# Performance work log

Hardware: AMD Instinct MI355X
Metric: run time of the kernel (lower is better)

## Reference

```python
import jax, jax.numpy as jnp
import numpy as np

FFT_LIST = [32, 64, 128]
C_IN = 64
C_OUT = 96
C_OUT_PER = C_OUT // len(FFT_LIST)  # 32
BASIC = FFT_LIST[1]                 # base kernel defined at fft=64 -> 33 bins
ALPHA = 0.2                         # tf.nn.leaky_relu default


def setup_inputs() -> dict:
    key = jax.random.key(0)
    k1, k2, k3, k4 = jax.random.split(key, 4)
    B, T = 8, 8192
    bins0 = BASIC // 2 + 1
    return {
        "x": jax.random.normal(k1, (B, T, C_IN), dtype=jnp.float32),
        "kernel_r": jax.random.normal(k2, (1, 1, bins0, C_IN * C_OUT_PER), dtype=jnp.float32) * 0.05,
        "kernel_i": jax.random.normal(k3, (1, 1, bins0, C_IN * C_OUT_PER), dtype=jnp.float32) * 0.05,
        "bias_r": jax.random.normal(k4, (C_OUT,), dtype=jnp.float32) * 0.05,
    }


def _resize_bins(k, bins):
    # tf.image.resize on [1, H=1, W=bins0, C]: bilinear along W, half-pixel, no antialias
    if bins == k.shape[2]:
        return k
    return jax.image.resize(k, (1, 1, bins, k.shape[3]), method="linear", antialias=False)


def _leaky(v):
    return jax.nn.leaky_relu(v, negative_slope=ALPHA)


def reference(x, kernel_r, kernel_i, bias_r):
    B, T, _ = x.shape
    xc = jnp.transpose(x, (0, 2, 1))  # [B, C_in, T]
    outs = []
    for fft_n in FFT_LIST:
        frames = T // fft_n
        bins = fft_n // 2 + 1
        # non-overlapping STFT with no window == reshape + rfft
        xf = jnp.fft.rfft(xc.reshape(B, C_IN, frames, fft_n), axis=-1)  # [B, Cin, F, K] complex64
        kr = _resize_bins(kernel_r, bins)
        ki = _resize_bins(kernel_i, bins)
        kern = (kr + 1j * ki).reshape(bins, C_IN, C_OUT_PER).astype(jnp.complex64)  # [K, Cin, Cout]
        # per-frequency-bin complex matmul over c_in (fuses tile+mul+reduce_sum)
        y = jnp.einsum("bcfk,kco->bofk", xf, kern)  # [B, Cout, F, K]
        # act_domain == 'freq': leaky relu on real and imag parts
        y = _leaky(jnp.real(y)) + 1j * _leaky(jnp.imag(y))
        # inverse STFT (step == length, no window) == irfft + reshape
        yt = jnp.fft.irfft(y, n=fft_n, axis=-1)            # [B, Cout, F, fft_n]
        yt = yt.reshape(B, C_OUT_PER, T)                    # [B, Cout, T]
        outs.append(jnp.transpose(yt, (0, 2, 1)))           # [B, T, Cout]
    out = jnp.concatenate(outs, axis=2)                     # [B, T, C_OUT]
    out = out + bias_r                                      # bias_add(real(bias))
    return out
```

## Files before the change

kernel.cpp:

```cpp
#include <hip/hip_runtime.h>
#include <stdint.h>

#define T_SZ 8192
#define NCH 96

typedef __attribute__((ext_vector_type(8))) short s8v;
typedef __attribute__((ext_vector_type(4))) float f4v;

__device__ __forceinline__ float lo_bf(uint32_t u){ return __uint_as_float(u << 16); }
__device__ __forceinline__ float hi_bf(uint32_t u){ return __uint_as_float(u & 0xffff0000u); }
__device__ __forceinline__ uint32_t f2bf(float f){
    uint32_t u = __float_as_uint(f);
    return (u + 0x7fffu + ((u >> 16) & 1u)) >> 16;
}
__device__ __forceinline__ uint32_t pk2(float a, float b){ return f2bf(a) | (f2bf(b) << 16); }

#define WS_TOTAL_PAIRS 235520
#define WD_OFF    942080
#define WD_ELEMS  27264
#define WA_OFF    996608
#define WA_ELEMS  30464
#define WD64_U16   1920
#define WD128_U16  7680
#define WA64_U16   2304
#define WA128_U16  8960
#define WE_OFF   1057536
#define WE_U32    471040
#define XF32W    4194304
#define XF64W   14680064
#define XF128W  25165824
#define Y32W    35651584
#define Y64W    41943040
#define Y128W   50331648
#define WS_WIDE 58720256

__global__ void prep_full(const float* __restrict__ kr, const float* __restrict__ ki,
                          char* __restrict__ ws)
{
    int idx = blockIdx.x * 256 + threadIdx.x;
    if (idx < WE_U32) {
        int g = idx >> 12, r = idx & 4095;
        int row = r >> 6, c = r & 63;
        int o = row & 31, half = row >> 5;
        int bins, k;
        if (g < 17)      { bins = 17; k = g; }
        else if (g < 50) { bins = 33; k = g - 17; }
        else             { bins = 65; k = g - 50; }
        float s  = (k + 0.5f) * (33.0f / bins) - 0.5f;
        float fl = floorf(s);
        float w1 = s - fl;
        int i0 = min(max((int)fl, 0), 32);
        int i1 = min(max((int)fl + 1, 0), 32);
        int co = c * 32 + o;
        float r0 = kr[i0 * 2048 + co], r1 = kr[i1 * 2048 + co];
        float q0 = ki[i0 * 2048 + co], q1 = ki[i1 * 2048 + co];
        int N = bins * 2 - 2;
        float wk = (k == 0 || k == bins - 1) ? (1.0f / N) : (2.0f / N);
        float vr = fmaf(w1, r1 - r0, r0) * wk;
        float vi = fmaf(w1, q1 - q0, q0) * wk;
        ((uint32_t*)(ws + WE_OFF))[idx] = half ? pk2(vi, vr) : pk2(vr, -vi);
        return;
    }
    int e = idx - WE_U32;
    if (e < WD_ELEMS) {
        int N, NP, base;
        if (e < 1920)      { N = 32;  NP = 40;  base = 0; }
        else if (e < 7680) { N = 64;  NP = 72;  base = WD64_U16;  e -= 1920; }
        else               { N = 128; NP = 136; base = WD128_U16; e -= 7680; }
        int m = e / NP, t = e % NP;
        float v = 0.f;
        if (t < N && m < N + 2) {
            float ang = 6.2831853071795864769f * (float)(((m >> 1) * t) & (N - 1)) / (float)N;
            v = (m & 1) ? -sinf(ang) : cosf(ang);
        }
        ((unsigned short*)(ws + WD_OFF))[base + e] = (unsigned short)f2bf(v);
        return;
    }
    e -= WD_ELEMS;
    if (e < WA_ELEMS) {
        int N, S3, base;
        if (e < 2304)      { N = 32;  S3 = 72;  base = 0; }
        else if (e < 8960) { N = 64;  S3 = 104; base = WA64_U16;  e -= 2304; }
        else               { N = 128; S3 = 168; base = WA128_U16; e -= 8960; }
        int t = e / S3, kk = e % S3;
        int BINS = N / 2 + 1;
        float v = 0.f;
        if (kk < BINS)
            v = cosf(6.2831853071795864769f * (float)((kk * t) & (N - 1)) / (float)N);
        else if (kk < N + 2)
            v = -sinf(6.2831853071795864769f * (float)(((kk - BINS) * t) & (N - 1)) / (float)N);
        ((unsigned short*)(ws + WA_OFF))[base + e] = (unsigned short)f2bf(v);
    }
}

__global__ void prep_resize(const float* __restrict__ kr, const float* __restrict__ ki,
                            uint32_t* __restrict__ wsu)
{
    int idx = blockIdx.x * 256 + threadIdx.x;
    if (idx >= WS_TOTAL_PAIRS) return;
    int bins, rem = idx;
    if (rem < 17 * 2048)      { bins = 17; }
    else if (rem < 50 * 2048) { bins = 33; rem -= 17 * 2048; }
    else                      { bins = 65; rem -= 50 * 2048; }
    int k = rem >> 11, co = rem & 2047;
    float s  = (k + 0.5f) * (33.0f / bins) - 0.5f;
    float fl = floorf(s);
    float w1 = s - fl;
    int i0 = min(max((int)fl, 0), 32);
    int i1 = min(max((int)fl + 1, 0), 32);
    float r0 = kr[i0 * 2048 + co], r1 = kr[i1 * 2048 + co];
    float q0 = ki[i0 * 2048 + co], q1 = ki[i1 * 2048 + co];
    wsu[idx] = pk2(fmaf(w1, r1 - r0, r0), fmaf(w1, q1 - q0, q0));
}

__device__ __forceinline__ s8v ldfr(const unsigned short* p, int stride, int row0, int k0){
    int lane = threadIdx.x & 63;
    return *(const s8v*)(p + (row0 + (lane & 15)) * stride + k0 + ((lane >> 4) << 3));
}

template<int N, int NTW>
__device__ __forceinline__ void k1w_branch(const unsigned short* __restrict__ W,
        const unsigned short* __restrict__ xT, uint32_t* __restrict__ xfp, int b, int w)
{
    constexpr int BINS = N/2+1, M2 = 2*BINS, MPAD = ((M2+15)/16)*16;
    constexpr int MT = MPAD/16, KS = N/32, NP = N+8;
    constexpr int F = 128/N, FRAMES = 8192/N, BF = 8*FRAMES;
    const int tid = threadIdx.x, wv = tid >> 6, lane = tid & 63;
    const int nt0 = wv * NTW, cl = lane & 15, kl = (lane >> 4) << 3, rg = (lane >> 4) * 4;

    f4v acc[MT][NTW];
    #pragma unroll
    for (int mt = 0; mt < MT; ++mt)
        #pragma unroll
        for (int nw = 0; nw < NTW; ++nw) { f4v zz = {0.f,0.f,0.f,0.f}; acc[mt][nw] = zz; }

    for (int ks = 0; ks < KS; ++ks) {
        s8v a[MT];
        #pragma unroll
        for (int mt = 0; mt < MT; ++mt) a[mt] = ldfr(W, NP, mt*16, ks*32);
        #pragma unroll
        for (int nw = 0; nw < NTW; ++nw) {
            int rowb = (nt0+nw)*16 + cl;
            s8v bb = *(const s8v*)(xT + (rowb & 63)*136 + (rowb >> 6)*N + ks*32 + kl);
            #pragma unroll
            for (int mt = 0; mt < MT; ++mt)
                acc[mt][nw] = __builtin_amdgcn_mfma_f32_16x16x32_bf16(a[mt], bb, acc[mt][nw], 0, 0, 0);
        }
    }
    #pragma unroll
    for (int mt = 0; mt < MT; ++mt)
      #pragma unroll
      for (int nw = 0; nw < NTW; ++nw) {
        int col = (nt0+nw)*16 + cl, f = col >> 6, c = col & 63;
        size_t bf = (size_t)b*FRAMES + w*F + f;
        #pragma unroll
        for (int r = 0; r < 4; r += 2) {
            int m = mt*16 + rg + r, k = m >> 1;
            if (k < BINS)
                xfp[((size_t)k*BF + bf)*64 + c] = pk2(acc[mt][nw][r], acc[mt][nw][r+1]);
        }
      }
}

__global__ __launch_bounds__(256, 2) void k1w(const float* __restrict__ x, char* __restrict__ ws)
{
    __shared__ __align__(16) char smem[71936];
    unsigned short* xT   = (unsigned short*)smem;
    unsigned short* Wall = xT + 64*136;
    const unsigned short* WD = (const unsigned short*)(ws + WD_OFF);
    const int tid = threadIdx.x, bid = blockIdx.x;
    const int b = bid >> 6, w = bid & 63;

    for (int e = tid; e < WD_ELEMS/8; e += 256)
        *(uint4*)(Wall + e*8) = *(const uint4*)(WD + e*8);

    const float* xb = x + ((size_t)b*T_SZ + (size_t)w*128) * 64;
    for (int e = tid; e < 512; e += 256) {
        int c4 = e & 15, t0 = (e >> 4) * 4;
        const float* p = xb + (size_t)t0*64 + c4*4;
        float4 v0 = *(const float4*)(p);
        float4 v1 = *(const float4*)(p + 64);
        float4 v2 = *(const float4*)(p + 128);
        float4 v3 = *(const float4*)(p + 192);
        unsigned short* d = xT + (c4*4)*136 + t0;
        *(uint2*)(d)       = make_uint2(pk2(v0.x, v1.x), pk2(v2.x, v3.x));
        *(uint2*)(d + 136) = make_uint2(pk2(v0.y, v1.y), pk2(v2.y, v3.y));
        *(uint2*)(d + 272) = make_uint2(pk2(v0.z, v1.z), pk2(v2.z, v3.z));
        *(uint2*)(d + 408) = make_uint2(pk2(v0.w, v1.w), pk2(v2.w, v3.w));
    }
    __syncthreads();

    k1w_branch<32, 4>(Wall,             xT, (uint32_t*)(ws + XF32W),  b, w);
    k1w_branch<64, 2>(Wall + WD64_U16,  xT, (uint32_t*)(ws + XF64W),  b, w);
    k1w_branch<128,1>(Wall + WD128_U16, xT, (uint32_t*)(ws + XF128W), b, w);
}

template<int N>
__device__ __forceinline__ void k2_body(int kbin, int mblk, char* smem,
        const unsigned short* __restrict__ we, const uint32_t* __restrict__ xfp,
        unsigned short* __restrict__ y2)
{
    constexpr int BINS = N/2+1, FRAMES = 8192/N, BF = 8*FRAMES, M2 = 2*BINS;
    constexpr int GOFF = (N==32) ? 0 : (N==64) ? 17 : 50;
    unsigned short* A  = (unsigned short*)smem;
    unsigned short* W2 = A + 128*136;
    const int tid = threadIdx.x;
    const int bf0 = mblk * 128;

    for (int e = tid; e < 2048; e += 256)
        *(uint4*)(A + (e>>4)*136 + (e&15)*8) =
            *((const uint4*)(xfp + ((size_t)kbin*BF + bf0 + (e>>4))*64) + (e & 15));

    const uint4* wsrc = (const uint4*)(we + (size_t)(GOFF + kbin) * 8192);
    for (int e = tid; e < 1024; e += 256)
        *(uint4*)(W2 + (e>>4)*136 + (e&15)*8) = wsrc[e];
    __syncthreads();

    const int wv = tid >> 6, lane = tid & 63;
    const int mt0 = wv * 2;
    f4v acc[2][4];
    #pragma unroll
    for (int mt = 0; mt < 2; ++mt)
        #pragma unroll
        for (int nt = 0; nt < 4; ++nt) { f4v zz = {0.f,0.f,0.f,0.f}; acc[mt][nt] = zz; }

    for (int ks = 0; ks < 4; ++ks) {
        s8v a0 = ldfr(A, 136, mt0*16, ks*32);
        s8v a1 = ldfr(A, 136, mt0*16 + 16, ks*32);
        #pragma unroll
        for (int nt = 0; nt < 4; ++nt) {
            s8v bb = ldfr(W2, 136, nt*16, ks*32);
            acc[0][nt] = __builtin_amdgcn_mfma_f32_16x16x32_bf16(a0, bb, acc[0][nt], 0, 0, 0);
            acc[1][nt] = __builtin_amdgcn_mfma_f32_16x16x32_bf16(a1, bb, acc[1][nt], 0, 0, 0);
        }
    }
    const int cl = lane & 15, rg = (lane >> 4) * 4;
    #pragma unroll
    for (int mt = 0; mt < 2; ++mt)
      #pragma unroll
      for (int nt = 0; nt < 4; ++nt) {
        int col = nt*16 + cl;
        int kk = (col < 32) ? kbin : BINS + kbin;
        int o = col & 31;
        #pragma unroll
        for (int r = 0; r < 4; ++r) {
            int bf = bf0 + (mt0+mt)*16 + rg + r;
            float v = acc[mt][nt][r];
            v = (v > 0.f) ? v : 0.2f * v;
            y2[((size_t)bf*M2 + kk)*32 + o] = (unsigned short)f2bf(v);
        }
      }
}

__global__ __launch_bounds__(256, 3) void k2all(char* __restrict__ ws)
{
    __shared__ __align__(16) char smem[52224];
    const unsigned short* we = (const unsigned short*)(ws + WE_OFF);
    int bid = blockIdx.x;
    if (bid < 272)
        k2_body<32>(bid >> 4, bid & 15, smem, we,
                    (const uint32_t*)(ws + XF32W), (unsigned short*)(ws + Y32W));
    else if (bid < 536) {
        int q = bid - 272;
        k2_body<64>(q >> 3, q & 7, smem, we,
                    (const uint32_t*)(ws + XF64W), (unsigned short*)(ws + Y64W));
    } else {
        int q = bid - 536;
        k2_body<128>(q >> 2, q & 3, smem, we,
                     (const uint32_t*)(ws + XF128W), (unsigned short*)(ws + Y128W));
    }
}

template<int N, int TROWS>
__device__ __forceinline__ void k3_body(int b, int f0, int t0, char* smem,
        const unsigned short* __restrict__ WA, const unsigned short* __restrict__ y2,
        const float* __restrict__ bias, float* __restrict__ out)
{
    constexpr int BINS = N/2+1, FRAMES = 8192/N, M2 = 2*BINS;
    constexpr int KP = ((M2+31)/32)*32, S3 = KP+8, KS = KP/32;
    constexpr int FB = (N==32)?8:(N==64)?4:2;
    constexpr int COFF = (N==32)?0:(N==64)?32:64;
    constexpr int NTW = (N==128)?4:8;

    unsigned short* A  = (unsigned short*)smem;
    unsigned short* Bt = A + TROWS*S3;
    const int tid = threadIdx.x;

    for (int e = tid; e < TROWS*S3/8; e += 256)
        *(uint4*)(A + e*8) = *(const uint4*)(WA + t0*S3 + e*8);

    for (int e = tid; e < FB*M2*4; e += 256) {
        int f = e / (M2*4), r = e % (M2*4), kk = r >> 2, og = (r & 3)*8;
        size_t bf = (size_t)b*FRAMES + f0 + f;
        uint4 v = *((const uint4*)(y2 + ((size_t)bf*M2 + kk)*32) + (r & 3));
        unsigned short* dst = Bt + (f*32 + og)*S3 + kk;
        const unsigned short* pv = (const unsigned short*)&v;
        #pragma unroll
        for (int j = 0; j < 8; ++j) dst[j*S3] = pv[j];
    }
    __syncthreads();

    const int wv = tid >> 6, lane = tid & 63;
    const int mt0 = (N==32) ? (wv & 1) : wv;
    const int nt0 = (N==32) ? (wv >> 1)*8 : 0;

    f4v acc[NTW];
    #pragma unroll
    for (int nw = 0; nw < NTW; ++nw) { f4v zz = {0.f,0.f,0.f,0.f}; acc[nw] = zz; }

    for (int ks = 0; ks < KS; ++ks) {
        s8v a = ldfr(A, S3, mt0*16, ks*32);
        #pragma unroll
        for (int nw = 0; nw < NTW; ++nw) {
            s8v bb = ldfr(Bt, S3, (nt0+nw)*16, ks*32);
            acc[nw] = __builtin_amdgcn_mfma_f32_16x16x32_bf16(a, bb, acc[nw], 0, 0, 0);
        }
    }
    const int cl = lane & 15, rg = (lane >> 4) * 4;
    #pragma unroll
    for (int nw = 0; nw < NTW; ++nw) {
        int col = (nt0+nw)*16 + cl, f = col >> 5, o = col & 31;
        float bv = bias[COFF + o];
        #pragma unroll
        for (int r = 0; r < 4; ++r) {
            int t = t0 + mt0*16 + rg + r;
            out[((size_t)(b*T_SZ + (f0+f)*N + t))*NCH + COFF + o] = acc[nw][r] + bv;
        }
    }
}

__global__ __launch_bounds__(256, 3) void k3all(char* __restrict__ ws,
        const float* __restrict__ bias, float* __restrict__ out)
{
    __shared__ __align__(16) char smem[43008];
    const unsigned short* WA = (const unsigned short*)(ws + WA_OFF);
    int bid = blockIdx.x;
    if (bid < 256)
        k3_body<32,32>(bid >> 5, (bid & 31)*8, 0, smem, WA,
                       (const unsigned short*)(ws + Y32W), bias, out);
    else if (bid < 512) {
        int q = bid - 256;
        k3_body<64,64>(q >> 5, (q & 31)*4, 0, smem, WA + WA64_U16,
                       (const unsigned short*)(ws + Y64W), bias, out);
    } else {
        int q = bid - 512;
        k3_body<128,64>(q >> 6, ((q & 63) >> 1)*2, (q & 1)*64, smem, WA + WA128_U16,
                        (const unsigned short*)(ws + Y128W), bias, out);
    }
}

template<int FFT_N, bool USE_WS>
__global__ __launch_bounds__(256, 2)
void stft_fused(const float* __restrict__ x, const float* __restrict__ kr,
                const float* __restrict__ ki, const float* __restrict__ bias,
                const uint32_t* __restrict__ wsu, float* __restrict__ out)
{
    constexpr int CIN = 64, COUT = 32;
    constexpr int BINS = FFT_N / 2 + 1;
    constexpr int NFR  = 128 / FFT_N;
    constexpr int KQ   = (BINS + 3) / 4;
    constexpr int COFF = (FFT_N == 32) ? 0 : (FFT_N == 64) ? 32 : 64;
    constexpr int WSP  = (FFT_N == 32) ? 0 : (FFT_N == 64) ? 17 * 2048 : 50 * 2048;
    constexpr int XSP  = 68;
    constexpr int CP   = 66;
    constexpr int YP   = BINS + 2;
    constexpr int SMEMF = 128 * XSP + 2 * FFT_N + NFR * BINS * CP * 2;

    __shared__ __align__(16) float smem[SMEMF];
    float*  xs  = smem;
    float2* cst = (float2*)(smem + 128 * XSP);
    float2* xf2 = (float2*)(smem + 128 * XSP + 2 * FFT_N);
    float2* Y2  = (float2*)smem;

    const int tid = threadIdx.x;
    const int bid = blockIdx.x;
    const int b = bid >> 6, w = bid & 63;
    const float* xblk = x + (size_t)(b * T_SZ + w * 128) * CIN;

    for (int i = tid; i < 2048; i += 256) {
        float4 v = ((const float4*)xblk)[i];
        int t = i >> 4;
        int c = (i & 15) * 4;
        *(float4*)&xs[t * XSP + c] = v;
    }
    if (tid < FFT_N) {
        float ang = 6.2831853071795864769f * ((float)tid / (float)FFT_N);
        float sv, cv;
        sincosf(ang, &sv, &cv);
        cst[tid] = make_float2(cv, sv);
    }
    __syncthreads();

    constexpr int NT_DFT = NFR * KQ * 16;
    for (int tile = tid; tile < NT_DFT; tile += 256) {
        int cq  = tile & 15;
        int kqf = tile >> 4;
        int kq  = kqf % KQ, f = kqf / KQ;
        int k0  = kq * 4;
        float accr[4][4] = {};
        float acci[4][4] = {};
        int idx[4] = {0, 0, 0, 0};
        const float* xrow = xs + f * FFT_N * XSP + cq * 4;
        for (int t = 0; t < FFT_N; ++t) {
            float4 xv = *(const float4*)(xrow + t * XSP);
            float xc[4] = {xv.x, xv.y, xv.z, xv.w};
            #pragma unroll
            for (int kk = 0; kk < 4; ++kk) {
                float2 tw = cst[idx[kk]];
                idx[kk] = (idx[kk] + k0 + kk) & (FFT_N - 1);
                #pragma unroll
                for (int cc = 0; cc < 4; ++cc) {
                    accr[kk][cc] = fmaf(xc[cc], tw.x, accr[kk][cc]);
                    acci[kk][cc] = fmaf(xc[cc], tw.y, acci[kk][cc]);
                }
            }
        }
        #pragma unroll
        for (int kk = 0; kk < 4; ++kk) {
            int k = k0 + kk;
            if (k < BINS) {
                #pragma unroll
                for (int cc = 0; cc < 4; ++cc)
                    xf2[(f * BINS + k) * CP + cq * 4 + cc] =
                        make_float2(accr[kk][cc], -acci[kk][cc]);
            }
        }
    }
    __syncthreads();

    constexpr int NT_MM = BINS * 8;
    for (int task = tid; task < NT_MM; task += 256) {
        int oq = task & 7, k = task >> 3;
        float2 accY[NFR][4] = {};
        float w1 = 0.f; int i0 = 0, i1 = 0;
        if (!USE_WS) {
            float s  = (k + 0.5f) * (33.0f / BINS) - 0.5f;
            float fl = floorf(s); w1 = s - fl;
            i0 = min(max((int)fl, 0), 32);
            i1 = min(max((int)fl + 1, 0), 32);
        }
        const uint32_t* wp = USE_WS ? (wsu + WSP + k * 2048 + oq * 4) : (const uint32_t*)nullptr;
        for (int c = 0; c < CIN; ++c) {
            float krv[4], kiv[4];
            if (USE_WS) {
                uint4 u = *(const uint4*)(wp + c * 32);
                krv[0] = lo_bf(u.x); kiv[0] = hi_bf(u.x);
                krv[1] = lo_bf(u.y); kiv[1] = hi_bf(u.y);
                krv[2] = lo_bf(u.z); kiv[2] = hi_bf(u.z);
                krv[3] = lo_bf(u.w); kiv[3] = hi_bf(u.w);
            } else {
                const float* p = kr + (size_t)i0 * 2048 + c * 32 + oq * 4;
                const float* q = kr + (size_t)i1 * 2048 + c * 32 + oq * 4;
                float4 r0 = *(const float4*)p, r1 = *(const float4*)q;
                p = ki + (size_t)i0 * 2048 + c * 32 + oq * 4;
                q = ki + (size_t)i1 * 2048 + c * 32 + oq * 4;
                float4 q0 = *(const float4*)p, q1 = *(const float4*)q;
                krv[0] = fmaf(w1, r1.x - r0.x, r0.x); kiv[0] = fmaf(w1, q1.x - q0.x, q0.x);
                krv[1] = fmaf(w1, r1.y - r0.y, r0.y); kiv[1] = fmaf(w1, q1.y - q0.y, q0.y);
                krv[2] = fmaf(w1, r1.z - r0.z, r0.z); kiv[2] = fmaf(w1, q1.z - q0.z, q0.z);
                krv[3] = fmaf(w1, r1.w - r0.w, r0.w); kiv[3] = fmaf(w1, q1.w - q0.w, q0.w);
            }
            #pragma unroll
            for (int f = 0; f < NFR; ++f) {
                float2 xv = xf2[(f * BINS + k) * CP + c];
                #pragma unroll
                for (int jo = 0; jo < 4; ++jo) {
                    accY[f][jo].x += xv.x * krv[jo] - xv.y * kiv[jo];
                    accY[f][jo].y += xv.x * kiv[jo] + xv.y * krv[jo];
                }
            }
        }
        float wk = (k == 0 || k == BINS - 1) ? (1.0f / FFT_N) : (2.0f / FFT_N);
        #pragma unroll
        for (int f = 0; f < NFR; ++f) {
            #pragma unroll
            for (int jo = 0; jo < 4; ++jo) {
                float yr = accY[f][jo].x; yr = (yr > 0.f) ? yr : 0.2f * yr;
                float yi = accY[f][jo].y; yi = (yi > 0.f) ? yi : 0.2f * yi;
                Y2[(f * COUT + oq * 4 + jo) * YP + k] = make_float2(yr * wk, yi * wk);
            }
        }
    }
    __syncthreads();

    {
        int tq = tid >> 3, oq = tid & 7;
        int tg0 = tq * 4;
        int f   = tg0 / FFT_N;
        int tl0 = tg0 % FFT_N;
        float acc[4][4] = {};
        int idx[4] = {0, 0, 0, 0};
        const float2* yb = Y2 + (f * COUT + oq * 4) * YP;
        for (int k = 0; k < BINS; ++k) {
            float2 tw[4];
            #pragma unroll
            for (int j = 0; j < 4; ++j) {
                tw[j] = cst[idx[j]];
                idx[j] = (idx[j] + tl0 + j) & (FFT_N - 1);
            }
            #pragma unroll
            for (int jo = 0; jo < 4; ++jo) {
                float2 yv = yb[jo * YP + k];
                #pragma unroll
                for (int j = 0; j < 4; ++j)
                    acc[j][jo] += yv.x * tw[j].x - yv.y * tw[j].y;
            }
        }
        float4 bv = *(const float4*)(bias + COFF + oq * 4);
        float* ob = out + ((size_t)(b * T_SZ + w * 128 + tg0)) * NCH + COFF + oq * 4;
        #pragma unroll
        for (int j = 0; j < 4; ++j) {
            float4 o4 = make_float4(acc[j][0] + bv.x, acc[j][1] + bv.y,
                                    acc[j][2] + bv.z, acc[j][3] + bv.w);
            *(float4*)(ob + (size_t)j * NCH) = o4;
        }
    }
}

extern "C" void kernel_launch(void* const* d_in, const int* in_sizes, int n_in,
                              void* d_out, int out_size, void* d_ws, size_t ws_size,
                              hipStream_t stream)
{
    (void)in_sizes; (void)n_in; (void)out_size;
    const float* x    = (const float*)d_in[0];
    const float* kr   = (const float*)d_in[1];
    const float* ki   = (const float*)d_in[2];
    const float* bias = (const float*)d_in[3];
    float* out = (float*)d_out;
    char* ws = (char*)d_ws;
    dim3 blk(256);

    if (ws != nullptr && ws_size >= (size_t)WS_WIDE) {
        prep_full<<<dim3(2066), blk, 0, stream>>>(kr, ki, ws);
        k1w   <<<dim3(512),  blk, 0, stream>>>(x, ws);
        k2all <<<dim3(796),  blk, 0, stream>>>(ws);
        k3all <<<dim3(1024), blk, 0, stream>>>(ws, bias, out);
    } else if (ws != nullptr && ws_size >= (size_t)WS_TOTAL_PAIRS * 4) {
        uint32_t* wsu = (uint32_t*)ws;
        prep_resize<<<dim3(920), blk, 0, stream>>>(kr, ki, wsu);
        stft_fused<32,  true><<<dim3(512), blk, 0, stream>>>(x, kr, ki, bias, wsu, out);
        stft_fused<64,  true><<<dim3(512), blk, 0, stream>>>(x, kr, ki, bias, wsu, out);
        stft_fused<128, true><<<dim3(512), blk, 0, stream>>>(x, kr, ki, bias, wsu, out);
    } else {
        stft_fused<32,  false><<<dim3(512), blk, 0, stream>>>(x, kr, ki, bias, nullptr, out);
        stft_fused<64,  false><<<dim3(512), blk, 0, stream>>>(x, kr, ki, bias, nullptr, out);
        stft_fused<128, false><<<dim3(512), blk, 0, stream>>>(x, kr, ki, bias, nullptr, out);
    }
}
```

Measured before the change: 50.37 us.

## Fuse kernel resize into k2, widen k1w to 512 threads, interleave re/im layout

```diff
diff --git a/kernel.cpp b/kernel.cpp
--- a/kernel.cpp
+++ b/kernel.cpp
@@ -24,8 +24,6 @@
 #define WD128_U16  7680
 #define WA64_U16   2304
 #define WA128_U16  8960
-#define WE_OFF   1057536
-#define WE_U32    471040
 #define XF32W    4194304
 #define XF64W   14680064
 #define XF128W  25165824
@@ -34,34 +32,9 @@
 #define Y128W   50331648
 #define WS_WIDE 58720256
 
-__global__ void prep_full(const float* __restrict__ kr, const float* __restrict__ ki,
-                          char* __restrict__ ws)
-{
-    int idx = blockIdx.x * 256 + threadIdx.x;
-    if (idx < WE_U32) {
-        int g = idx >> 12, r = idx & 4095;
-        int row = r >> 6, c = r & 63;
-        int o = row & 31, half = row >> 5;
-        int bins, k;
-        if (g < 17)      { bins = 17; k = g; }
-        else if (g < 50) { bins = 33; k = g - 17; }
-        else             { bins = 65; k = g - 50; }
-        float s  = (k + 0.5f) * (33.0f / bins) - 0.5f;
-        float fl = floorf(s);
-        float w1 = s - fl;
-        int i0 = min(max((int)fl, 0), 32);
-        int i1 = min(max((int)fl + 1, 0), 32);
-        int co = c * 32 + o;
-        float r0 = kr[i0 * 2048 + co], r1 = kr[i1 * 2048 + co];
-        float q0 = ki[i0 * 2048 + co], q1 = ki[i1 * 2048 + co];
-        int N = bins * 2 - 2;
-        float wk = (k == 0 || k == bins - 1) ? (1.0f / N) : (2.0f / N);
-        float vr = fmaf(w1, r1 - r0, r0) * wk;
-        float vi = fmaf(w1, q1 - q0, q0) * wk;
-        ((uint32_t*)(ws + WE_OFF))[idx] = half ? pk2(vi, vr) : pk2(vr, -vi);
-        return;
-    }
-    int e = idx - WE_U32;
+__global__ void prep_full(char* __restrict__ ws)
+{
+    int e = blockIdx.x * 256 + threadIdx.x;
     if (e < WD_ELEMS) {
         int N, NP, base;
         if (e < 1920)      { N = 32;  NP = 40;  base = 0; }
@@ -83,12 +56,13 @@
         else if (e < 8960) { N = 64;  S3 = 104; base = WA64_U16;  e -= 2304; }
         else               { N = 128; S3 = 168; base = WA128_U16; e -= 8960; }
         int t = e / S3, kk = e % S3;
-        int BINS = N / 2 + 1;
+        int M2 = N + 2;
         float v = 0.f;
-        if (kk < BINS)
-            v = cosf(6.2831853071795864769f * (float)((kk * t) & (N - 1)) / (float)N);
-        else if (kk < N + 2)
-            v = -sinf(6.2831853071795864769f * (float)(((kk - BINS) * t) & (N - 1)) / (float)N);
+        if (kk < M2) {
+            int k = kk >> 1;
+            float ang = 6.2831853071795864769f * (float)((k * t) & (N - 1)) / (float)N;
+            v = (kk & 1) ? -sinf(ang) : cosf(ang);
+        }
         ((unsigned short*)(ws + WA_OFF))[base + e] = (unsigned short)f2bf(v);
     }
 }
@@ -118,51 +92,51 @@
     return *(const s8v*)(p + (row0 + (lane & 15)) * stride + k0 + ((lane >> 4) << 3));
 }
 
-template<int N, int NTW>
+template<int N, int NTW, int MT0, int MTN>
 __device__ __forceinline__ void k1w_branch(const unsigned short* __restrict__ W,
-        const unsigned short* __restrict__ xT, uint32_t* __restrict__ xfp, int b, int w)
-{
-    constexpr int BINS = N/2+1, M2 = 2*BINS, MPAD = ((M2+15)/16)*16;
-    constexpr int MT = MPAD/16, KS = N/32, NP = N+8;
-    constexpr int F = 128/N, FRAMES = 8192/N, BF = 8*FRAMES;
-    const int tid = threadIdx.x, wv = tid >> 6, lane = tid & 63;
-    const int nt0 = wv * NTW, cl = lane & 15, kl = (lane >> 4) << 3, rg = (lane >> 4) * 4;
-
-    f4v acc[MT][NTW];
+        const unsigned short* __restrict__ xT, uint32_t* __restrict__ xfp,
+        int b, int w, int nt0)
+{
+    constexpr int BINS = N/2+1, KS = N/32, NP = N+8;
+    constexpr int F = 128/N, FRAMES = 8192/N;
+    const int lane = threadIdx.x & 63;
+    const int cl = lane & 15, kl = (lane >> 4) << 3, rg = (lane >> 4) * 4;
+
+    f4v acc[MTN][NTW];
     #pragma unroll
-    for (int mt = 0; mt < MT; ++mt)
+    for (int mt = 0; mt < MTN; ++mt)
         #pragma unroll
         for (int nw = 0; nw < NTW; ++nw) { f4v zz = {0.f,0.f,0.f,0.f}; acc[mt][nw] = zz; }
 
     for (int ks = 0; ks < KS; ++ks) {
-        s8v a[MT];
-        #pragma unroll
-        for (int mt = 0; mt < MT; ++mt) a[mt] = ldfr(W, NP, mt*16, ks*32);
+        s8v a[MTN];
+        #pragma unroll
+        for (int mt = 0; mt < MTN; ++mt) a[mt] = ldfr(W, NP, (MT0+mt)*16, ks*32);
         #pragma unroll
         for (int nw = 0; nw < NTW; ++nw) {
             int rowb = (nt0+nw)*16 + cl;
             s8v bb = *(const s8v*)(xT + (rowb & 63)*136 + (rowb >> 6)*N + ks*32 + kl);
             #pragma unroll
-            for (int mt = 0; mt < MT; ++mt)
+            for (int mt = 0; mt < MTN; ++mt)
                 acc[mt][nw] = __builtin_amdgcn_mfma_f32_16x16x32_bf16(a[mt], bb, acc[mt][nw], 0, 0, 0);
         }
     }
     #pragma unroll
-    for (int mt = 0; mt < MT; ++mt)
+    for (int mt = 0; mt < MTN; ++mt)
       #pragma unroll
       for (int nw = 0; nw < NTW; ++nw) {
         int col = (nt0+nw)*16 + cl, f = col >> 6, c = col & 63;
         size_t bf = (size_t)b*FRAMES + w*F + f;
         #pragma unroll
         for (int r = 0; r < 4; r += 2) {
-            int m = mt*16 + rg + r, k = m >> 1;
+            int m = (MT0+mt)*16 + rg + r, k = m >> 1;
             if (k < BINS)
-                xfp[((size_t)k*BF + bf)*64 + c] = pk2(acc[mt][nw][r], acc[mt][nw][r+1]);
+                xfp[((size_t)k*(8*FRAMES) + bf)*64 + c] = pk2(acc[mt][nw][r], acc[mt][nw][r+1]);
         }
       }
 }
 
-__global__ __launch_bounds__(256, 2) void k1w(const float* __restrict__ x, char* __restrict__ ws)
+__global__ __launch_bounds__(512, 4) void k1w(const float* __restrict__ x, char* __restrict__ ws)
 {
     __shared__ __align__(16) char smem[71936];
     unsigned short* xT   = (unsigned short*)smem;
@@ -171,11 +145,12 @@
     const int tid = threadIdx.x, bid = blockIdx.x;
     const int b = bid >> 6, w = bid & 63;
 
-    for (int e = tid; e < WD_ELEMS/8; e += 256)
+    for (int e = tid; e < WD_ELEMS/8; e += 512)
         *(uint4*)(Wall + e*8) = *(const uint4*)(WD + e*8);
 
     const float* xb = x + ((size_t)b*T_SZ + (size_t)w*128) * 64;
-    for (int e = tid; e < 512; e += 256) {
+    {
+        int e = tid;
         int c4 = e & 15, t0 = (e >> 4) * 4;
         const float* p = xb + (size_t)t0*64 + c4*4;
         float4 v0 = *(const float4*)(p);
@@ -190,18 +165,21 @@
     }
     __syncthreads();
 
-    k1w_branch<32, 4>(Wall,             xT, (uint32_t*)(ws + XF32W),  b, w);
-    k1w_branch<64, 2>(Wall + WD64_U16,  xT, (uint32_t*)(ws + XF64W),  b, w);
-    k1w_branch<128,1>(Wall + WD128_U16, xT, (uint32_t*)(ws + XF128W), b, w);
+    const int wv = tid >> 6;
+    k1w_branch<32, 2, 0, 3>(Wall,             xT, (uint32_t*)(ws + XF32W),  b, w, wv*2);
+    k1w_branch<64, 1, 0, 5>(Wall + WD64_U16,  xT, (uint32_t*)(ws + XF64W),  b, w, wv);
+    if (wv < 4)
+        k1w_branch<128, 1, 0, 5>(Wall + WD128_U16, xT, (uint32_t*)(ws + XF128W), b, w, wv);
+    else
+        k1w_branch<128, 1, 5, 4>(Wall + WD128_U16, xT, (uint32_t*)(ws + XF128W), b, w, wv & 3);
 }
 
 template<int N>
 __device__ __forceinline__ void k2_body(int kbin, int mblk, char* smem,
-        const unsigned short* __restrict__ we, const uint32_t* __restrict__ xfp,
-        unsigned short* __restrict__ y2)
-{
-    constexpr int BINS = N/2+1, FRAMES = 8192/N, BF = 8*FRAMES, M2 = 2*BINS;
-    constexpr int GOFF = (N==32) ? 0 : (N==64) ? 17 : 50;
+        const float* __restrict__ kr, const float* __restrict__ ki,
+        const uint32_t* __restrict__ xfp, uint32_t* __restrict__ y2p)
+{
+    constexpr int BINS = N/2+1, FRAMES = 8192/N, BF = 8*FRAMES;
     unsigned short* A  = (unsigned short*)smem;
     unsigned short* W2 = A + 128*136;
     const int tid = threadIdx.x;
@@ -211,9 +189,25 @@
         *(uint4*)(A + (e>>4)*136 + (e&15)*8) =
             *((const uint4*)(xfp + ((size_t)kbin*BF + bf0 + (e>>4))*64) + (e & 15));
 
-    const uint4* wsrc = (const uint4*)(we + (size_t)(GOFF + kbin) * 8192);
-    for (int e = tid; e < 1024; e += 256)
-        *(uint4*)(W2 + (e>>4)*136 + (e&15)*8) = wsrc[e];
+    {
+        float s  = (kbin + 0.5f) * (33.0f / BINS) - 0.5f;
+        float fl = floorf(s);
+        float w1 = s - fl;
+        int i0 = min(max((int)fl, 0), 32);
+        int i1 = min(max((int)fl + 1, 0), 32);
+        float wk = (kbin == 0 || kbin == BINS-1) ? (1.0f/N) : (2.0f/N);
+        for (int e = tid; e < 2048; e += 256) {
+            float r0 = kr[i0*2048 + e], r1 = kr[i1*2048 + e];
+            float q0 = ki[i0*2048 + e], q1 = ki[i1*2048 + e];
+            float vr = fmaf(w1, r1 - r0, r0) * wk;
+            float vi = fmaf(w1, q1 - q0, q0) * wk;
+            int c = e >> 5, o = e & 31;
+            W2[o*136 + 2*c]          = (unsigned short)f2bf(vr);
+            W2[o*136 + 2*c + 1]      = (unsigned short)f2bf(-vi);
+            W2[(32+o)*136 + 2*c]     = (unsigned short)f2bf(vi);
+            W2[(32+o)*136 + 2*c + 1] = (unsigned short)f2bf(vr);
+        }
+    }
     __syncthreads();
 
     const int wv = tid >> 6, lane = tid & 63;
@@ -238,47 +232,46 @@
     #pragma unroll
     for (int mt = 0; mt < 2; ++mt)
       #pragma unroll
-      for (int nt = 0; nt < 4; ++nt) {
-        int col = nt*16 + cl;
-        int kk = (col < 32) ? kbin : BINS + kbin;
-        int o = col & 31;
+      for (int nt = 0; nt < 2; ++nt) {
+        int o = nt*16 + cl;
         #pragma unroll
         for (int r = 0; r < 4; ++r) {
             int bf = bf0 + (mt0+mt)*16 + rg + r;
-            float v = acc[mt][nt][r];
-            v = (v > 0.f) ? v : 0.2f * v;
-            y2[((size_t)bf*M2 + kk)*32 + o] = (unsigned short)f2bf(v);
+            float re = acc[mt][nt][r];   re = (re > 0.f) ? re : 0.2f * re;
+            float im = acc[mt][nt+2][r]; im = (im > 0.f) ? im : 0.2f * im;
+            y2p[((size_t)bf*BINS + kbin)*32 + o] = pk2(re, im);
         }
       }
 }
 
-__global__ __launch_bounds__(256, 3) void k2all(char* __restrict__ ws)
+__global__ __launch_bounds__(256, 3) void k2all(const float* __restrict__ kr,
+        const float* __restrict__ ki, char* __restrict__ ws)
 {
     __shared__ __align__(16) char smem[52224];
-    const unsigned short* we = (const unsigned short*)(ws + WE_OFF);
     int bid = blockIdx.x;
     if (bid < 272)
-        k2_body<32>(bid >> 4, bid & 15, smem, we,
-                    (const uint32_t*)(ws + XF32W), (unsigned short*)(ws + Y32W));
+        k2_body<32>(bid >> 4, bid & 15, smem, kr, ki,
+                    (const uint32_t*)(ws + XF32W), (uint32_t*)(ws + Y32W));
     else if (bid < 536) {
         int q = bid - 272;
-        k2_body<64>(q >> 3, q & 7, smem, we,
-                    (const uint32_t*)(ws + XF64W), (unsigned short*)(ws + Y64W));
+        k2_body<64>(q >> 3, q & 7, smem, kr, ki,
+                    (const uint32_t*)(ws + XF64W), (uint32_t*)(ws + Y64W));
     } else {
         int q = bid - 536;
-        k2_body<128>(q >> 2, q & 3, smem, we,
-                     (const uint32_t*)(ws + XF128W), (unsigned short*)(ws + Y128W));
+        k2_body<128>(q >> 2, q & 3, smem, kr, ki,
+                     (const uint32_t*)(ws + XF128W), (uint32_t*)(ws + Y128W));
     }
 }
 
 template<int N, int TROWS>
 __device__ __forceinline__ void k3_body(int b, int f0, int t0, char* smem,
-        const unsigned short* __restrict__ WA, const unsigned short* __restrict__ y2,
+        const unsigned short* __restrict__ WA, const uint32_t* __restrict__ y2p,
         const float* __restrict__ bias, float* __restrict__ out)
 {
     constexpr int BINS = N/2+1, FRAMES = 8192/N, M2 = 2*BINS;
     constexpr int KP = ((M2+31)/32)*32, S3 = KP+8, KS = KP/32;
     constexpr int FB = (N==32)?8:(N==64)?4:2;
+    constexpr int NCOLS = FB*32;
     constexpr int COFF = (N==32)?0:(N==64)?32:64;
     constexpr int NTW = (N==128)?4:8;
 
@@ -289,14 +282,15 @@
     for (int e = tid; e < TROWS*S3/8; e += 256)
         *(uint4*)(A + e*8) = *(const uint4*)(WA + t0*S3 + e*8);
 
-    for (int e = tid; e < FB*M2*4; e += 256) {
-        int f = e / (M2*4), r = e % (M2*4), kk = r >> 2, og = (r & 3)*8;
+    for (int e = tid; e < FB*BINS*32; e += 256) {
+        int o = e & 31, k = (e >> 5) % BINS, f = e / (32*BINS);
         size_t bf = (size_t)b*FRAMES + f0 + f;
-        uint4 v = *((const uint4*)(y2 + ((size_t)bf*M2 + kk)*32) + (r & 3));
-        unsigned short* dst = Bt + (f*32 + og)*S3 + kk;
-        const unsigned short* pv = (const unsigned short*)&v;
-        #pragma unroll
-        for (int j = 0; j < 8; ++j) dst[j*S3] = pv[j];
+        uint32_t v = y2p[(bf*BINS + k)*32 + o];
+        *(uint32_t*)(Bt + (f*32 + o)*S3 + 2*k) = v;
+    }
+    for (int e = tid; e < NCOLS*15; e += 256) {
+        int row = e / 15, j = e % 15;
+        *(uint32_t*)(Bt + row*S3 + M2 + 2*j) = 0u;
     }
     __syncthreads();
 
@@ -337,15 +331,15 @@
     int bid = blockIdx.x;
     if (bid < 256)
         k3_body<32,32>(bid >> 5, (bid & 31)*8, 0, smem, WA,
-                       (const unsigned short*)(ws + Y32W), bias, out);
+                       (const uint32_t*)(ws + Y32W), bias, out);
     else if (bid < 512) {
         int q = bid - 256;
         k3_body<64,64>(q >> 5, (q & 31)*4, 0, smem, WA + WA64_U16,
-                       (const unsigned short*)(ws + Y64W), bias, out);
+                       (const uint32_t*)(ws + Y64W), bias, out);
     } else {
         int q = bid - 512;
         k3_body<128,64>(q >> 6, ((q & 63) >> 1)*2, (q & 1)*64, smem, WA + WA128_U16,
-                        (const unsigned short*)(ws + Y128W), bias, out);
+                        (const uint32_t*)(ws + Y128W), bias, out);
     }
 }
 
@@ -531,9 +525,9 @@
     dim3 blk(256);
 
     if (ws != nullptr && ws_size >= (size_t)WS_WIDE) {
-        prep_full<<<dim3(2066), blk, 0, stream>>>(kr, ki, ws);
-        k1w   <<<dim3(512),  blk, 0, stream>>>(x, ws);
-        k2all <<<dim3(796),  blk, 0, stream>>>(ws);
+        prep_full<<<dim3(226), blk, 0, stream>>>(ws);
+        k1w   <<<dim3(512),  dim3(512), 0, stream>>>(x, ws);
+        k2all <<<dim3(796),  blk, 0, stream>>>(kr, ki, ws);
         k3all <<<dim3(1024), blk, 0, stream>>>(ws, bias, out);
     } else if (ws != nullptr && ws_size >= (size_t)WS_TOTAL_PAIRS * 4) {
         uint32_t* wsu = (uint32_t*)ws;
```

New measurement: 48.13 us. 4.4% less time.
